# Performance work log

Measured on AMD Instinct MI355X. Metric: run time of the kernel, lower is better.

Reference implementation:

```python
import jax, jax.numpy as jnp
import numpy as np


def setup_inputs() -> dict:
    key = jax.random.key(0)
    k1, k2 = jax.random.split(key)
    q, k, d5 = 128, 2048, 768
    return {
        "tgt": jax.random.normal(k1, (q, d5), dtype=jnp.float32),
        "memory": jax.random.normal(k2, (k, d5), dtype=jnp.float32),
        "seq_len": 32,
    }


def reference(tgt, memory, seq_len):
    q, d5 = tgt.shape
    k, _ = memory.shape
    z = d5 // seq_len  # per-token sub-dim
    query_t = tgt.reshape(q, seq_len, z)    # [q, t, d]
    key_m = memory.reshape(k, seq_len, z)   # [k, s, d]
    # Full late-interaction similarity tensor [q, k, s, t]
    score = jnp.einsum('qtd,ksd->qkst', query_t, key_m)
    # max over memory tokens (s) and over query tokens (t), concat, mean
    pooled = jnp.concatenate((score.max(axis=2), score.max(axis=3)), axis=-1)  # [q, k, 2*seq_len]
    score_p = jax.nn.sigmoid(pooled.mean(axis=-1))  # [q, k]
    return (score_p, score_p)
```

## Files before the change

kernel.cpp:

```cpp
#include <hip/hip_runtime.h>
#include <hip/hip_bf16.h>

typedef __bf16 bf16x8 __attribute__((ext_vector_type(8)));
typedef short  s16x4  __attribute__((ext_vector_type(4)));
typedef float  f32x16 __attribute__((ext_vector_type(16)));

constexpr int QN  = 128;
constexpr int KN  = 2048;
constexpr int D5  = 768;
constexpr int SL  = 32;
constexpr int ZD  = 24;
constexpr int KCH = 16;

#if __has_builtin(__builtin_amdgcn_mfma_f32_32x32x8bf16_1k)
#define HAVE_MFMA_X8 1
#else
#define HAVE_MFMA_X8 0
#endif

static __device__ __forceinline__ float max3f(float a, float b, float c) {
    return fmaxf(fmaxf(a, b), c);
}

static __device__ __forceinline__ float redmax16(const f32x16& a) {
    float x0 = max3f(a[0],  a[1],  a[2]);
    float x1 = max3f(a[3],  a[4],  a[5]);
    float x2 = max3f(a[6],  a[7],  a[8]);
    float x3 = max3f(a[9],  a[10], a[11]);
    float x4 = max3f(a[12], a[13], a[14]);
    float y0 = max3f(x0, x1, x2);
    float y1 = max3f(x3, x4, a[15]);
    return fmaxf(y0, y1);
}

#if HAVE_MFMA_X8
static __device__ __forceinline__ short f2bfbits(float x) {
    __bf16 b = (__bf16)x;
    return __builtin_bit_cast(short, b);
}
#endif

__global__ __launch_bounds__(256, 4) void matcher_kernel(const float* __restrict__ tgt,
                                                         const float* __restrict__ mem,
                                                         float* __restrict__ out)
{
    __shared__ __align__(16) __bf16 Kf[KCH * 768];
    __shared__ float vbuf[4][KCH * 32];

    const int tid = threadIdx.x;
    const int kc  = blockIdx.x;
    const int qg  = blockIdx.y;
    const int k0  = kc * KCH;

    for (int r = tid; r < KCH * SL; r += 256) {
        const int kl = r >> 5;
        const int s  = r & 31;
        const float* src = mem + (size_t)(k0 + kl) * D5 + s * ZD;
        float tv[24];
#pragma unroll
        for (int j = 0; j < 6; ++j) ((float4*)tv)[j] = ((const float4*)src)[j];
        bf16x8 a, b, c;
#pragma unroll
        for (int j = 0; j < 8; ++j) {
            a[j] = (__bf16)tv[j];
            b[j] = (__bf16)tv[8 + j];
            c[j] = (__bf16)tv[16 + j];
        }
        __bf16* base = Kf + kl * 768;
        *(bf16x8*)(base +        s * 8)  = a;
        *(bf16x8*)(base + (32 +  s) * 8) = b;
        *(bf16x8*)(base + 512 +  s * 8)  = c;
    }

    const int lane = tid & 63;
    const int wv   = tid >> 6;
    const int t    = lane & 31;
    const int h    = lane >> 5;
    const int q    = qg * 4 + wv;

    const float4* p4 = (const float4*)(tgt + (size_t)q * D5 + t * ZD);
    bf16x8 aQ0;
    {
        float4 u0 = p4[2 * h], u1 = p4[2 * h + 1];
        aQ0[0] = (__bf16)u0.x; aQ0[1] = (__bf16)u0.y; aQ0[2] = (__bf16)u0.z; aQ0[3] = (__bf16)u0.w;
        aQ0[4] = (__bf16)u1.x; aQ0[5] = (__bf16)u1.y; aQ0[6] = (__bf16)u1.z; aQ0[7] = (__bf16)u1.w;
    }
#if HAVE_MFMA_X8
    s16x4 aQ1;
    {
        float4 w = p4[4 + h];
        aQ1[0] = f2bfbits(w.x); aQ1[1] = f2bfbits(w.y);
        aQ1[2] = f2bfbits(w.z); aQ1[3] = f2bfbits(w.w);
    }
#else
    bf16x8 aQ1;
    if (h == 0) {
        float4 w0 = p4[4], w1 = p4[5];
        aQ1[0] = (__bf16)w0.x; aQ1[1] = (__bf16)w0.y; aQ1[2] = (__bf16)w0.z; aQ1[3] = (__bf16)w0.w;
        aQ1[4] = (__bf16)w1.x; aQ1[5] = (__bf16)w1.y; aQ1[6] = (__bf16)w1.z; aQ1[7] = (__bf16)w1.w;
    } else {
#pragma unroll
        for (int j = 0; j < 8; ++j) aQ1[j] = (__bf16)0.0f;
    }
#endif

    f32x16 zacc;
#pragma unroll
    for (int i = 0; i < 16; ++i) zacc[i] = 0.0f;
    asm volatile("" : "+v"(zacc));

    __syncthreads();

    float* vb = vbuf[wv];

#pragma unroll
    for (int kl = 0; kl < KCH; ++kl) {
        const __bf16* lb = Kf + kl * 768;
        bf16x8 bK0 = *(const bf16x8*)(lb + lane * 8);
#if HAVE_MFMA_X8
        s16x4 bK1 = *(const s16x4*)(lb + 512 + t * 8 + h * 4);

        f32x16 accS = __builtin_amdgcn_mfma_f32_32x32x16_bf16(aQ0, bK0, zacc, 0, 0, 0);
        accS = __builtin_amdgcn_mfma_f32_32x32x8bf16_1k(aQ1, bK1, accS, 0, 0, 0);
        f32x16 accT = __builtin_amdgcn_mfma_f32_32x32x16_bf16(bK0, aQ0, zacc, 0, 0, 0);
        accT = __builtin_amdgcn_mfma_f32_32x32x8bf16_1k(bK1, aQ1, accT, 0, 0, 0);
#else
        bf16x8 bK1 = *(const bf16x8*)(lb + 512 + t * 8);

        f32x16 accS = __builtin_amdgcn_mfma_f32_32x32x16_bf16(aQ0, bK0, zacc, 0, 0, 0);
        accS        = __builtin_amdgcn_mfma_f32_32x32x16_bf16(aQ1, bK1, accS, 0, 0, 0);
        f32x16 accT = __builtin_amdgcn_mfma_f32_32x32x16_bf16(bK0, aQ0, zacc, 0, 0, 0);
        accT        = __builtin_amdgcn_mfma_f32_32x32x16_bf16(bK1, aQ1, accT, 0, 0, 0);
#endif
        asm volatile("" : "+v"(accS), "+v"(accT));

        float m1 = redmax16(accS);
        float m2 = redmax16(accT);
        m1 = fmaxf(m1, __shfl_xor(m1, 32));
        m2 = fmaxf(m2, __shfl_xor(m2, 32));
        float v = m1 + m2;
        if (h == 0) vb[(kl << 5) + (t ^ kl)] = v;
    }

    {
        const int p    = lane & 15;
        const int half = (lane >> 4) & 1;
        float x[16];
#pragma unroll
        for (int i = 0; i < 16; ++i)
            x[i] = vb[(p << 5) + ((half << 4) + i ^ p)];
        float s0 = (x[0] + x[1]) + (x[2] + x[3]);
        float s1 = (x[4] + x[5]) + (x[6] + x[7]);
        float s2 = (x[8] + x[9]) + (x[10] + x[11]);
        float s3 = (x[12] + x[13]) + (x[14] + x[15]);
        float sum = (s0 + s1) + (s2 + s3);
        sum += __shfl_xor(sum, 16);
        float r = 1.0f / (1.0f + __expf(-sum * (1.0f / 64.0f)));
        if (lane < 16) {
            const int idx = q * KN + k0 + p;
            out[idx] = r;
            out[idx + QN * KN] = r;
        }
    }
}

extern "C" void kernel_launch(void* const* d_in, const int* in_sizes, int n_in,
                              void* d_out, int out_size, void* d_ws, size_t ws_size,
                              hipStream_t stream)
{
    const float* tgt = (const float*)d_in[0];
    const float* mem = (const float*)d_in[1];
    float* out = (float*)d_out;
    dim3 grid(KN / KCH, QN / 4);
    matcher_kernel<<<grid, 256, 0, stream>>>(tgt, mem, out);
}
```

Baseline: 94.40 us.

## Use 8-wave blocks, swap grid order, and use permlane32 swap for half-wave max

Blocks grow from 4 to 8 query waves, so each memory chunk staged in LDS serves twice as many queries and each thread converts exactly one memory row with no loop. The grid is transposed so adjacent blocks share the same memory chunk, which should improve L2 reuse. The cross-half max now uses permlane32_swap when available instead of a DS-based shuffle, and the asm barriers that pinned accumulators are removed, giving the compiler more freedom to schedule. Bigger blocks with launch_bounds(512,4) may raise register pressure or reduce scheduling flexibility.

Result: faster. 92.19 us (-2.3%).

```diff
diff --git a/kernel.cpp b/kernel.cpp
--- a/kernel.cpp
+++ b/kernel.cpp
@@ -4,6 +4,7 @@
 typedef __bf16 bf16x8 __attribute__((ext_vector_type(8)));
 typedef short  s16x4  __attribute__((ext_vector_type(4)));
 typedef float  f32x16 __attribute__((ext_vector_type(16)));
+typedef int    i32x2  __attribute__((ext_vector_type(2)));
 
 constexpr int QN  = 128;
 constexpr int KN  = 2048;
@@ -11,11 +12,18 @@
 constexpr int SL  = 32;
 constexpr int ZD  = 24;
 constexpr int KCH = 16;
+constexpr int WPB = 8;
 
 #if __has_builtin(__builtin_amdgcn_mfma_f32_32x32x8bf16_1k)
 #define HAVE_MFMA_X8 1
 #else
 #define HAVE_MFMA_X8 0
+#endif
+
+#if __has_builtin(__builtin_amdgcn_permlane32_swap)
+#define HAVE_PERMLANE32 1
+#else
+#define HAVE_PERMLANE32 0
 #endif
 
 static __device__ __forceinline__ float max3f(float a, float b, float c) {
@@ -33,6 +41,17 @@
     return fmaxf(y0, y1);
 }
 
+static __device__ __forceinline__ float halfmax(float m) {
+#if HAVE_PERMLANE32
+    i32x2 pr = __builtin_amdgcn_permlane32_swap(__builtin_bit_cast(int, m),
+                                                __builtin_bit_cast(int, m),
+                                                false, false);
+    return fmaxf(__builtin_bit_cast(float, pr[0]), __builtin_bit_cast(float, pr[1]));
+#else
+    return fmaxf(m, __shfl_xor(m, 32));
+#endif
+}
+
 #if HAVE_MFMA_X8
 static __device__ __forceinline__ short f2bfbits(float x) {
     __bf16 b = (__bf16)x;
@@ -40,19 +59,20 @@
 }
 #endif
 
-__global__ __launch_bounds__(256, 4) void matcher_kernel(const float* __restrict__ tgt,
+__global__ __launch_bounds__(512, 4) void matcher_kernel(const float* __restrict__ tgt,
                                                          const float* __restrict__ mem,
                                                          float* __restrict__ out)
 {
     __shared__ __align__(16) __bf16 Kf[KCH * 768];
-    __shared__ float vbuf[4][KCH * 32];
+    __shared__ float vbuf[WPB][KCH * 32];
 
     const int tid = threadIdx.x;
-    const int kc  = blockIdx.x;
-    const int qg  = blockIdx.y;
+    const int qg  = blockIdx.x;
+    const int kc  = blockIdx.y;
     const int k0  = kc * KCH;
 
-    for (int r = tid; r < KCH * SL; r += 256) {
+    {
+        const int r  = tid;
         const int kl = r >> 5;
         const int s  = r & 31;
         const float* src = mem + (size_t)(k0 + kl) * D5 + s * ZD;
@@ -76,7 +96,7 @@
     const int wv   = tid >> 6;
     const int t    = lane & 31;
     const int h    = lane >> 5;
-    const int q    = qg * 4 + wv;
+    const int q    = qg * WPB + wv;
 
     const float4* p4 = (const float4*)(tgt + (size_t)q * D5 + t * ZD);
     bf16x8 aQ0;
@@ -107,7 +127,6 @@
     f32x16 zacc;
 #pragma unroll
     for (int i = 0; i < 16; ++i) zacc[i] = 0.0f;
-    asm volatile("" : "+v"(zacc));
 
     __syncthreads();
 
@@ -132,12 +151,8 @@
         f32x16 accT = __builtin_amdgcn_mfma_f32_32x32x16_bf16(bK0, aQ0, zacc, 0, 0, 0);
         accT        = __builtin_amdgcn_mfma_f32_32x32x16_bf16(bK1, aQ1, accT, 0, 0, 0);
 #endif
-        asm volatile("" : "+v"(accS), "+v"(accT));
-
-        float m1 = redmax16(accS);
-        float m2 = redmax16(accT);
-        m1 = fmaxf(m1, __shfl_xor(m1, 32));
-        m2 = fmaxf(m2, __shfl_xor(m2, 32));
+        float m1 = halfmax(redmax16(accS));
+        float m2 = halfmax(redmax16(accT));
         float v = m1 + m2;
         if (h == 0) vb[(kl << 5) + (t ^ kl)] = v;
     }
@@ -171,6 +186,6 @@
     const float* tgt = (const float*)d_in[0];
     const float* mem = (const float*)d_in[1];
     float* out = (float*)d_out;
-    dim3 grid(KN / KCH, QN / 4);
-    matcher_kernel<<<grid, 256, 0, stream>>>(tgt, mem, out);
+    dim3 grid(QN / WPB, KN / KCH);
+    matcher_kernel<<<grid, 512, 0, stream>>>(tgt, mem, out);
 }
```
